# Optimization experiments

Measured on AMD Instinct MI355X. Metric: run time of the kernel, lower is better.

The kernel has to match this reference:

```python
import jax, jax.numpy as jnp
import numpy as np
from jax import lax

NX, NY = 6, 6
NB = NX * NY            # 36 blocks
B, S = 64, 256          # batch, sample_count
EPS = 1e-6

def build_edges(nx, ny):
    edges = []
    for i in range(nx):
        for j in range(ny):
            for dx, dy in [(-1, 0), (0, -1), (0, 1), (1, 0)]:
                x, y = i + dx, j + dy
                if 0 <= x < nx and 0 <= y < ny:
                    edges.append((j * nx + i, y * nx + x))
    return np.array(edges, np.int32)   # (120, 2)

EDGES_NP = build_edges(NX, NY)
NE = len(EDGES_NP)  # 120

def setup_inputs() -> dict:
    key = jax.random.key(0)
    ks = jax.random.split(key, 24)
    f32 = jnp.float32
    d = {
        "image":      jax.random.normal(ks[0], (B, 1, 32, 32), f32),
        "edge_noise": jax.random.uniform(ks[1], (B, S, NE), f32),
        "u_s":        jax.random.uniform(ks[2], (B, S, NB), f32),
        "u_d":        jax.random.uniform(ks[3], (B, S, NB), f32),
        # CNN params (OIHW)
        "cw1": jax.random.normal(ks[4], (32, 1, 5, 5), f32) * 0.05,
        "cb1": jnp.zeros((32,), f32),
        "cw2": jax.random.normal(ks[5], (32, 32, 5, 5), f32) * 0.05,
        "cb2": jnp.zeros((32,), f32),
        "cw3": jax.random.normal(ks[6], (64, 32, 5, 5), f32) * 0.05,
        "cb3": jnp.zeros((64,), f32),
        "cw4": jax.random.normal(ks[7], (64, 64, 5, 5), f32) * 0.05,
        "cb4": jnp.zeros((64,), f32),
        # is_connected MLP
        "wc1": jax.random.normal(ks[8], (256, 256), f32) * 0.05,
        "bc1": jnp.zeros((256,), f32),
        "wc2": jax.random.normal(ks[9], (256, NE), f32) * 0.05,
        "bc2": jnp.zeros((NE,), f32),
        # is_endpoint MLP
        "we1": jax.random.normal(ks[10], (256, 256), f32) * 0.05,
        "be1": jnp.zeros((256,), f32),
        "we2": jax.random.normal(ks[11], (256, NB), f32) * 0.05,
        "be2": jnp.zeros((NB,), f32),
        "edges": jnp.asarray(EDGES_NP),  # (NE, 2) int32, constants
    }
    return d

def _conv(x, w, b):
    y = lax.conv_general_dilated(x, w, (1, 1), 'VALID',
                                 dimension_numbers=('NCHW', 'OIHW', 'NCHW'))
    return y + b[None, :, None, None]

def _pool2(x):
    return lax.reduce_window(x, -jnp.inf, lax.max, (1, 1, 2, 2), (1, 1, 2, 2), 'VALID')

def reference(image, edge_noise, u_s, u_d,
              cw1, cb1, cw2, cb2, cw3, cb3, cw4, cb4,
              wc1, bc1, wc2, bc2, we1, be1, we2, be2, edges):
    # ---- CNN feature extractor ----
    h = _conv(image, cw1, cb1)
    h = _conv(h, cw2, cb2)
    h = _pool2(h)
    h = _conv(h, cw3, cb3)
    h = _conv(h, cw4, cb4)
    h = _pool2(h)
    emb = h.reshape(h.shape[0], -1)              # (B, 256)

    # ---- heads ----
    p_conn = jax.nn.sigmoid(jax.nn.relu(emb @ wc1 + bc1) @ wc2 + bc2)   # (B, NE)
    p_ep   = jax.nn.sigmoid(jax.nn.relu(emb @ we1 + be1) @ we2 + be2)   # (B, NB)

    pc = jnp.clip(p_conn, EPS, 1.0 - EPS)
    pe = jnp.clip(p_ep, EPS, 1.0 - EPS)
    cat = pe / pe.sum(-1, keepdims=True)
    logcat = jnp.log(cat)                        # (B, NB)

    # ---- Monte-Carlo sampling (ISED blackbox) ----
    conn = (edge_noise < pc[:, None, :]).astype(pc.dtype)               # (B,S,NE) Bernoulli
    g_s = -jnp.log(-jnp.log(jnp.clip(u_s, EPS, 1.0 - EPS)))
    g_d = -jnp.log(-jnp.log(jnp.clip(u_d, EPS, 1.0 - EPS)))
    s_idx = jnp.argmax(logcat[:, None, :] + g_s, axis=-1)               # (B,S) categorical
    d_idx = jnp.argmax(logcat[:, None, :] + g_d, axis=-1)               # (B,S)

    # ---- batched BFS reachability via boolean matrix squaring ----
    oh_u = jax.nn.one_hot(edges[:, 0], NB, dtype=pc.dtype)              # (NE, NB)
    oh_v = jax.nn.one_hot(edges[:, 1], NB, dtype=pc.dtype)
    e_sym = jnp.einsum('eu,ev->euv', oh_u, oh_v) + jnp.einsum('eu,ev->evu', oh_u, oh_v)
    A = jnp.minimum(jnp.einsum('bse,euv->bsuv', conn, e_sym), 1.0)      # (B,S,36,36)

    R = jnp.minimum(A + jnp.eye(NB, dtype=A.dtype), 1.0)
    for _ in range(6):                           # (I+A)^(2^6), covers path len<=36
        R = jnp.minimum(R @ R, 1.0)
    P = jnp.minimum(A @ R, 1.0)                  # paths of length >= 1 (BFS semantics)

    Pv = jnp.take_along_axis(P, s_idx[:, :, None, None], axis=2)[:, :, 0, :]  # (B,S,36)
    exists = (jnp.take_along_axis(Pv, d_idx[:, :, None], axis=2)[:, :, 0] > 0.5).astype(pc.dtype)  # (B,S)

    # ---- sample-probability weighting (differentiable ISED estimator) ----
    logw = (conn * jnp.log(pc)[:, None, :] + (1.0 - conn) * jnp.log1p(-pc)[:, None, :]).sum(-1)
    logw = logw + jnp.take_along_axis(logcat, s_idx, axis=1) \
                + jnp.take_along_axis(logcat, d_idx, axis=1)            # (B,S)
    w = jax.nn.softmax(logw, axis=1)
    p1 = (w * exists).sum(axis=1)                # P(path exists)
    return jnp.stack([1.0 - p1, p1], axis=-1)    # (B, 2)
```

## Files before the change

kernel.cpp:

```cpp
#include <hip/hip_runtime.h>

typedef unsigned long long u64;
#define EPSF 1e-6f

__global__ __launch_bounds__(512) void k_conv1(const float* __restrict__ img,
                                               const float* __restrict__ cw1,
                                               const float* __restrict__ cb1,
                                               float* __restrict__ c1) {
  int slab = blockIdx.x, b = blockIdx.y;
  __shared__ float simg[32 * 33];
  for (int k = threadIdx.x; k < 1024; k += 512) {
    int y = k >> 5, x = k & 31;
    simg[y * 33 + x] = img[b * 1024 + k];
  }
  int half = threadIdx.x >> 8;
  int u = threadIdx.x & 255;
  int ocl = u >> 5;
  int x = u & 31;
  int oc = slab * 8 + ocl;
  int y0 = half * 14;
  float w[25];
#pragma unroll
  for (int k = 0; k < 25; ++k) w[k] = cw1[oc * 25 + k];
  float bias = cb1[oc];
  __syncthreads();
  if (x < 28) {
    float acc[5];
#pragma unroll
    for (int k = 0; k < 5; ++k) acc[k] = bias;
    float* outp = c1 + (b * 32 + oc) * 784 + x;
#pragma unroll
    for (int rr = 0; rr < 18; ++rr) {
      int r = y0 + rr;
      float in[5];
#pragma unroll
      for (int c = 0; c < 5; ++c) in[c] = simg[r * 33 + x + c];
#pragma unroll
      for (int ky = 0; ky < 5; ++ky) {
        if (rr < ky || rr - ky > 13) continue;
        int slot = (rr - ky) % 5;
#pragma unroll
        for (int kx = 0; kx < 5; ++kx)
          acc[slot] = fmaf(w[ky * 5 + kx], in[kx], acc[slot]);
      }
      if (rr >= 4) {
        int slot = (rr - 4) % 5;
        outp[(y0 + rr - 4) * 28] = acc[slot];
        acc[slot] = bias;
      }
    }
  }
}

__global__ __launch_bounds__(1024, 4) void k_conv2(const float* __restrict__ c1,
                                                   const float* __restrict__ cw2,
                                                   const float* __restrict__ cb2,
                                                   float* __restrict__ p1w) {
  int ocq = blockIdx.x, b = blockIdx.y;
  __shared__ float smem[32384];
  float* w2s = smem + 25984;
  int t = threadIdx.x;
  {
    const float4* src = (const float4*)(cw2 + ocq * 8 * 800);
    for (int k4 = t; k4 < 1600; k4 += 1024) {
      float4 v = src[k4];
      float vv[4] = {v.x, v.y, v.z, v.w};
      int k = k4 * 4;
#pragma unroll
      for (int r = 0; r < 4; ++r) {
        int kk = k + r;
        int o = kk / 800, rest = kk % 800;
        w2s[rest * 8 + o] = vv[r];
      }
    }
  }
  if (t < 784) {
    int row = t / 28, col = t % 28;
    int lofs = row * 29 + col;
    const float* src = c1 + (size_t)b * 25088 + t;
#pragma unroll
    for (int ic = 0; ic < 32; ++ic) smem[ic * 812 + lofs] = src[ic * 784];
  }
  int w = __builtin_amdgcn_readfirstlane(t >> 6);
  int ocg = w & 1;
  int icq = w >> 1;
  int l = t & 63;
  int py = l >> 3, px = l & 7;
  int oc0 = ocq * 8 + ocg * 4;
  float acc[4][9];
#pragma unroll
  for (int o = 0; o < 4; ++o)
#pragma unroll
    for (int e = 0; e < 9; ++e) acc[o][e] = 0.f;
  __syncthreads();

  const float* base0 = smem + icq * 4 * 812 + (3 * py) * 29 + 3 * px;
  const float* wk0 = w2s + icq * 800 + ocg * 4;
#pragma unroll
  for (int icl = 0; icl < 4; ++icl) {
    const float* base = base0 + icl * 812;
    float win[7][7];
#pragma unroll
    for (int rr = 0; rr < 7; ++rr)
#pragma unroll
      for (int m = 0; m < 7; ++m) win[rr][m] = base[rr * 29 + m];
    const float* wk = wk0 + icl * 200;
#pragma unroll
    for (int ky = 0; ky < 5; ++ky) {
      float wq[5][4];
#pragma unroll
      for (int kx = 0; kx < 5; ++kx)
        *(float4*)wq[kx] = *(const float4*)(wk + (ky * 5 + kx) * 8);
#pragma unroll
      for (int i = 0; i < 3; ++i) {
#pragma unroll
        for (int kx = 0; kx < 5; ++kx) {
#pragma unroll
          for (int jj = 0; jj < 3; ++jj) {
            float v = win[i + ky][jj + kx];
            acc[0][i * 3 + jj] = fmaf(wq[kx][0], v, acc[0][i * 3 + jj]);
            acc[1][i * 3 + jj] = fmaf(wq[kx][1], v, acc[1][i * 3 + jj]);
            acc[2][i * 3 + jj] = fmaf(wq[kx][2], v, acc[2][i * 3 + jj]);
            acc[3][i * 3 + jj] = fmaf(wq[kx][3], v, acc[3][i * 3 + jj]);
          }
        }
      }
    }
  }

  __syncthreads();
  float* slots = smem;
  float* cbuf = smem + 18432;
  int chunk = ocg * 2304 + l * 9;
  if (icq >= 4) {
    float* d = slots + (icq - 4) * 4608 + chunk;
#pragma unroll
    for (int o = 0; o < 4; ++o)
#pragma unroll
      for (int e = 0; e < 9; ++e) d[o * 576 + e] = acc[o][e];
  }
  __syncthreads();
  if (icq < 4) {
    const float* s = slots + icq * 4608 + chunk;
#pragma unroll
    for (int o = 0; o < 4; ++o)
#pragma unroll
      for (int e = 0; e < 9; ++e) acc[o][e] += s[o * 576 + e];
  }
  __syncthreads();
  if (icq == 2 || icq == 3) {
    float* d = slots + (icq - 2) * 4608 + chunk;
#pragma unroll
    for (int o = 0; o < 4; ++o)
#pragma unroll
      for (int e = 0; e < 9; ++e) d[o * 576 + e] = acc[o][e];
  }
  __syncthreads();
  if (icq < 2) {
    const float* s = slots + icq * 4608 + chunk;
#pragma unroll
    for (int o = 0; o < 4; ++o)
#pragma unroll
      for (int e = 0; e < 9; ++e) acc[o][e] += s[o * 576 + e];
  }
  __syncthreads();
  if (icq == 1) {
    float* d = slots + chunk;
#pragma unroll
    for (int o = 0; o < 4; ++o)
#pragma unroll
      for (int e = 0; e < 9; ++e) d[o * 576 + e] = acc[o][e];
  }
  __syncthreads();
  if (icq == 0) {
    const float* s = slots + chunk;
#pragma unroll
    for (int o = 0; o < 4; ++o) {
      float bias = cb2[oc0 + o];
#pragma unroll
      for (int i = 0; i < 3; ++i)
#pragma unroll
        for (int jj = 0; jj < 3; ++jj)
          cbuf[(ocg * 4 + o) * 576 + (3 * py + i) * 24 + 3 * px + jj] =
              acc[o][i * 3 + jj] + s[o * 576 + i * 3 + jj] + bias;
    }
  }
  __syncthreads();
  for (int k = t; k < 1152; k += 1024) {
    int o = k / 144, rem = k % 144;
    int PY = rem / 12, PX = rem % 12;
    const float* b0 = cbuf + o * 576 + (2 * PY) * 24 + 2 * PX;
    float m = fmaxf(fmaxf(b0[0], b0[1]), fmaxf(b0[24], b0[25]));
    p1w[((size_t)b * 32 + ocq * 8 + o) * 144 + PY * 12 + PX] = m;
  }
}

__global__ __launch_bounds__(256) void k_conv3(const float* __restrict__ p1w,
                                               const float* __restrict__ cw3,
                                               const float* __restrict__ cb3,
                                               float* __restrict__ c3) {
  int oc8 = blockIdx.x, b = blockIdx.y;
  __shared__ float smem[11008];
  float* w3s = smem;
  float* ins = smem + 6400;
  int t = threadIdx.x;
  {
    const float4* src = (const float4*)(p1w + b * 32 * 144);
    float4* dst = (float4*)ins;
    for (int k = t; k < 1152; k += 256) dst[k] = src[k];
  }
  {
    const float4* src = (const float4*)(cw3 + oc8 * 8 * 800);
    for (int k4 = t; k4 < 1600; k4 += 256) {
      float4 v = src[k4];
      float vv[4] = {v.x, v.y, v.z, v.w};
      int k = k4 * 4;
#pragma unroll
      for (int r = 0; r < 4; ++r) {
        int kk = k + r;
        int o = kk / 800, rest = kk % 800;
        w3s[rest * 8 + o] = vv[r];
      }
    }
  }
  int g = t >> 4, p = t & 15;
  int ocg = p >> 3, row = p & 7;
  float acc[4][8];
#pragma unroll
  for (int j = 0; j < 4; ++j)
#pragma unroll
    for (int c = 0; c < 8; ++c) acc[j][c] = 0.f;
  __syncthreads();
#pragma unroll
  for (int icl = 0; icl < 2; ++icl) {
    int ic = g + icl * 16;
#pragma unroll
    for (int ky = 0; ky < 5; ++ky) {
      const float4* rp = (const float4*)(ins + ic * 144 + (row + ky) * 12);
      float win[12];
#pragma unroll
      for (int q = 0; q < 3; ++q) {
        float4 v = rp[q];
        win[4 * q] = v.x; win[4 * q + 1] = v.y; win[4 * q + 2] = v.z; win[4 * q + 3] = v.w;
      }
      const float* wb = w3s + (ic * 25 + ky * 5) * 8 + ocg * 4;
#pragma unroll
      for (int kx = 0; kx < 5; ++kx) {
        float wq[4];
        *(float4*)wq = *(const float4*)(wb + kx * 8);
#pragma unroll
        for (int c = 0; c < 8; ++c) {
#pragma unroll
          for (int j = 0; j < 4; ++j) acc[j][c] = fmaf(wq[j], win[c + kx], acc[j][c]);
        }
      }
    }
  }
  float* buf = smem;
  __syncthreads();
  if (g >= 8) {
    float* d = buf + (g - 8) * 512 + p * 32;
#pragma unroll
    for (int j = 0; j < 4; ++j)
#pragma unroll
      for (int c = 0; c < 8; ++c) d[j * 8 + c] = acc[j][c];
  }
  __syncthreads();
  if (g < 8) {
    const float* s = buf + g * 512 + p * 32;
#pragma unroll
    for (int j = 0; j < 4; ++j)
#pragma unroll
      for (int c = 0; c < 8; ++c) acc[j][c] += s[j * 8 + c];
  }
  __syncthreads();
  if (g >= 4 && g < 8) {
    float* d = buf + (g - 4) * 512 + p * 32;
#pragma unroll
    for (int j = 0; j < 4; ++j)
#pragma unroll
      for (int c = 0; c < 8; ++c) d[j * 8 + c] = acc[j][c];
  }
  __syncthreads();
  if (g < 4) {
    const float* s = buf + g * 512 + p * 32;
#pragma unroll
    for (int j = 0; j < 4; ++j)
#pragma unroll
      for (int c = 0; c < 8; ++c) acc[j][c] += s[j * 8 + c];
  }
  __syncthreads();
  if (g == 2 || g == 3) {
    float* d = buf + (g - 2) * 512 + p * 32;
#pragma unroll
    for (int j = 0; j < 4; ++j)
#pragma unroll
      for (int c = 0; c < 8; ++c) d[j * 8 + c] = acc[j][c];
  }
  __syncthreads();
  if (g < 2) {
    const float* s = buf + g * 512 + p * 32;
#pragma unroll
    for (int j = 0; j < 4; ++j)
#pragma unroll
      for (int c = 0; c < 8; ++c) acc[j][c] += s[j * 8 + c];
  }
  __syncthreads();
  if (g == 1) {
    float* d = buf + p * 32;
#pragma unroll
    for (int j = 0; j < 4; ++j)
#pragma unroll
      for (int c = 0; c < 8; ++c) d[j * 8 + c] = acc[j][c];
  }
  __syncthreads();
  if (g == 0) {
    const float* s = buf + p * 32;
#pragma unroll
    for (int j = 0; j < 4; ++j) {
      float bias = cb3[oc8 * 8 + ocg * 4 + j];
      float4 v0, v1;
      v0.x = acc[j][0] + s[j * 8 + 0] + bias; v0.y = acc[j][1] + s[j * 8 + 1] + bias;
      v0.z = acc[j][2] + s[j * 8 + 2] + bias; v0.w = acc[j][3] + s[j * 8 + 3] + bias;
      v1.x = acc[j][4] + s[j * 8 + 4] + bias; v1.y = acc[j][5] + s[j * 8 + 5] + bias;
      v1.z = acc[j][6] + s[j * 8 + 6] + bias; v1.w = acc[j][7] + s[j * 8 + 7] + bias;
      float* op = c3 + (b * 64 + oc8 * 8 + ocg * 4 + j) * 64 + row * 8;
      *(float4*)op = v0; *(float4*)(op + 4) = v1;
    }
  }
}

__global__ __launch_bounds__(256) void k_conv4(const float* __restrict__ c3,
                                               const float* __restrict__ cw4,
                                               const float* __restrict__ cb4,
                                               float* __restrict__ emb) {
  int oc8 = blockIdx.x, b = blockIdx.y;
  __shared__ float smem[17152];
  float* w4s = smem;
  float* ins = smem + 12800;
  int t = threadIdx.x;
  {
    const float4* src = (const float4*)(c3 + b * 4096);
    for (int k = t; k < 1024; k += 256) {
      int ic = k >> 4, q = k & 15;
      *(float4*)(ins + ic * 68 + q * 4) = src[k];
    }
  }
  {
    const float4* src = (const float4*)(cw4 + oc8 * 8 * 1600);
    for (int k4 = t; k4 < 3200; k4 += 256) {
      float4 v = src[k4];
      float vv[4] = {v.x, v.y, v.z, v.w};
      int k = k4 * 4;
#pragma unroll
      for (int r = 0; r < 4; ++r) {
        int kk = k + r;
        int o = kk / 1600, rest = kk % 1600;
        w4s[rest * 8 + o] = vv[r];
      }
    }
  }
  int g = t >> 3, p = t & 7;
  int ocg = p >> 2, row = p & 3;
  float acc[4][4];
#pragma unroll
  for (int j = 0; j < 4; ++j)
#pragma unroll
    for (int c = 0; c < 4; ++c) acc[j][c] = 0.f;
  __syncthreads();
#pragma unroll
  for (int icl = 0; icl < 2; ++icl) {
    int ic = g + icl * 32;
#pragma unroll
    for (int ky = 0; ky < 5; ++ky) {
      const float4* rp = (const float4*)(ins + ic * 68 + (row + ky) * 8);
      float win[8];
#pragma unroll
      for (int q = 0; q < 2; ++q) {
        float4 v = rp[q];
        win[4 * q] = v.x; win[4 * q + 1] = v.y; win[4 * q + 2] = v.z; win[4 * q + 3] = v.w;
      }
      const float* wb = w4s + (ic * 25 + ky * 5) * 8 + ocg * 4;
#pragma unroll
      for (int kx = 0; kx < 5; ++kx) {
        float wq[4];
        *(float4*)wq = *(const float4*)(wb + kx * 8);
#pragma unroll
        for (int c = 0; c < 4; ++c) {
#pragma unroll
          for (int j = 0; j < 4; ++j) acc[j][c] = fmaf(wq[j], win[c + kx], acc[j][c]);
        }
      }
    }
  }
  float* buf = smem;
#pragma unroll
  for (int half = 16; half >= 1; half >>= 1) {
    __syncthreads();
    if (g >= half && g < 2 * half) {
      float* d = buf + (g - half) * 128 + p * 16;
#pragma unroll
      for (int j = 0; j < 4; ++j)
#pragma unroll
        for (int c = 0; c < 4; ++c) d[j * 4 + c] = acc[j][c];
    }
    __syncthreads();
    if (g < half) {
      const float* s = buf + g * 128 + p * 16;
#pragma unroll
      for (int j = 0; j < 4; ++j)
#pragma unroll
        for (int c = 0; c < 4; ++c) acc[j][c] += s[j * 4 + c];
    }
  }
  float* pb = buf + 2048;
  if (g == 0) {
#pragma unroll
    for (int j = 0; j < 4; ++j) {
      float bias = cb4[oc8 * 8 + ocg * 4 + j];
#pragma unroll
      for (int c = 0; c < 4; ++c) pb[(ocg * 4 + j) * 16 + row * 4 + c] = acc[j][c] + bias;
    }
  }
  __syncthreads();
  if (t < 32) {
    int o = t >> 2, q = t & 3, py = q >> 1, px = q & 1;
    const float* b0 = pb + o * 16 + (2 * py) * 4 + 2 * px;
    float m = fmaxf(fmaxf(b0[0], b0[1]), fmaxf(b0[4], b0[5]));
    emb[b * 256 + (oc8 * 8 + o) * 4 + py * 2 + px] = m;
  }
}

__global__ __launch_bounds__(256) void k_heads(const float* __restrict__ emb,
    const float* __restrict__ wc1, const float* __restrict__ bc1,
    const float* __restrict__ wc2, const float* __restrict__ bc2,
    const float* __restrict__ we1, const float* __restrict__ be1,
    const float* __restrict__ we2, const float* __restrict__ be2,
    float* __restrict__ pcw, float* __restrict__ lpcw,
    float* __restrict__ l1mw, float* __restrict__ lcatw) {
  int head = blockIdx.x, b = blockIdx.y;
  int t = threadIdx.x;
  __shared__ float e_s[256], h_s[256];
  __shared__ float aux;
  e_s[t] = emb[b * 256 + t];
  __syncthreads();
  const float* W1 = head ? we1 : wc1;
  const float* B1 = head ? be1 : bc1;
  float s = B1[t];
  for (int i = 0; i < 256; i += 4) {
    s = fmaf(e_s[i], W1[i * 256 + t], s);
    s = fmaf(e_s[i + 1], W1[(i + 1) * 256 + t], s);
    s = fmaf(e_s[i + 2], W1[(i + 2) * 256 + t], s);
    s = fmaf(e_s[i + 3], W1[(i + 3) * 256 + t], s);
  }
  h_s[t] = fmaxf(s, 0.f);
  __syncthreads();
  int NO = head ? 36 : 120;
  const float* W2 = head ? we2 : wc2;
  const float* B2 = head ? be2 : bc2;
  if (t < NO) {
    float s2 = B2[t];
    for (int i = 0; i < 256; ++i) s2 = fmaf(h_s[i], W2[i * NO + t], s2);
    float p = 1.f / (1.f + expf(-s2));
    p = fminf(fmaxf(p, EPSF), 1.f - EPSF);
    if (head == 0) {
      pcw[b * 120 + t] = p;
      lpcw[b * 120 + t] = logf(p);
      l1mw[b * 120 + t] = log1pf(-p);
    } else {
      e_s[t] = p;
    }
  }
  if (head == 1) {
    __syncthreads();
    if (t == 0) {
      float sm = 0.f;
      for (int j2 = 0; j2 < 36; ++j2) sm += e_s[j2];
      aux = sm;
    }
    __syncthreads();
    if (t < 36) lcatw[b * 36 + t] = logf(e_s[t] / aux);
  }
}

__global__ __launch_bounds__(64) void k_mc1(const float* __restrict__ enoise,
    const float* __restrict__ us, const float* __restrict__ ud,
    const int* __restrict__ edges,
    const float* __restrict__ pcw, const float* __restrict__ lpcw,
    const float* __restrict__ l1mw, const float* __restrict__ lcatw,
    float* __restrict__ lw, float* __restrict__ exx) {
  int chunk = blockIdx.x, b = blockIdx.y, t = threadIdx.x;
  int s = chunk * 64 + t;
  __shared__ __align__(16) float pc_s[120];
  __shared__ __align__(16) float lpc_s[120];
  __shared__ __align__(16) float l1m_s[120];
  __shared__ __align__(16) float lcat_s[36];
  __shared__ __align__(16) int einfo[120];
  for (int k = t; k < 120; k += 64) {
    pc_s[k] = pcw[b * 120 + k];
    lpc_s[k] = lpcw[b * 120 + k];
    l1m_s[k] = l1mw[b * 120 + k];
    int u = edges[2 * k], v = edges[2 * k + 1];
    int d = v - u;
    int isV = (d == 6 || d == -6) ? 1 : 0;
    int pos = d > 0 ? u : v;
    einfo[k] = pos | (isV << 6);
  }
  if (t < 36) lcat_s[t] = lcatw[b * 36 + t];
  __syncthreads();

  float logw = 0.f;
  u64 H = 0, V = 0;
  {
    const float4* np = (const float4*)(enoise + ((size_t)(b * 256 + s)) * 120);
#pragma unroll
    for (int q = 0; q < 30; ++q) {
      float4 nz = np[q];
      float4 p4 = ((const float4*)pc_s)[q];
      float4 lp4 = ((const float4*)lpc_s)[q];
      float4 lm4 = ((const float4*)l1m_s)[q];
      int4 e4 = ((const int4*)einfo)[q];
      float nv[4] = {nz.x, nz.y, nz.z, nz.w};
      float pv[4] = {p4.x, p4.y, p4.z, p4.w};
      float lv[4] = {lp4.x, lp4.y, lp4.z, lp4.w};
      float mv[4] = {lm4.x, lm4.y, lm4.z, lm4.w};
      int ev[4] = {e4.x, e4.y, e4.z, e4.w};
#pragma unroll
      for (int r = 0; r < 4; ++r) {
        bool conn = nv[r] < pv[r];
        logw += conn ? lv[r] : mv[r];
        if (conn) {
          u64 bit = 1ull << (ev[r] & 63);
          if (ev[r] & 64) V |= bit; else H |= bit;
        }
      }
    }
  }
  int si = 0, di = 0;
  {
    const float4* up = (const float4*)(us + ((size_t)(b * 256 + s)) * 36);
    float best = -1e30f;
#pragma unroll
    for (int q = 0; q < 9; ++q) {
      float4 uv = up[q];
      float4 lc4 = ((const float4*)lcat_s)[q];
      float vv[4] = {uv.x, uv.y, uv.z, uv.w};
      float lc[4] = {lc4.x, lc4.y, lc4.z, lc4.w};
#pragma unroll
      for (int r = 0; r < 4; ++r) {
        float u = fminf(fmaxf(vv[r], EPSF), 1.f - EPSF);
        float gq = -logf(-logf(u));
        float val = lc[r] + gq;
        if (val > best) { best = val; si = q * 4 + r; }
      }
    }
  }
  {
    const float4* up = (const float4*)(ud + ((size_t)(b * 256 + s)) * 36);
    float best = -1e30f;
#pragma unroll
    for (int q = 0; q < 9; ++q) {
      float4 uv = up[q];
      float4 lc4 = ((const float4*)lcat_s)[q];
      float vv[4] = {uv.x, uv.y, uv.z, uv.w};
      float lc[4] = {lc4.x, lc4.y, lc4.z, lc4.w};
#pragma unroll
      for (int r = 0; r < 4; ++r) {
        float u = fminf(fmaxf(vv[r], EPSF), 1.f - EPSF);
        float gq = -logf(-logf(u));
        float val = lc[r] + gq;
        if (val > best) { best = val; di = q * 4 + r; }
      }
    }
  }
  logw += lcat_s[si] + lcat_s[di];

  u64 comp = 1ull << si;
  while (true) {
    u64 prev = comp;
    comp |= ((comp & H) << 1) | ((comp >> 1) & H);
    comp |= ((comp & V) << 6) | ((comp >> 6) & V);
    if (comp == prev) break;
  }
  float ex;
  if (si == di) ex = (comp != (1ull << si)) ? 1.f : 0.f;
  else ex = ((comp >> di) & 1ull) ? 1.f : 0.f;

  lw[b * 256 + s] = logw;
  exx[b * 256 + s] = ex;
}

__global__ __launch_bounds__(256) void k_mc2(const float* __restrict__ lw,
                                             const float* __restrict__ exx,
                                             float* __restrict__ out) {
  int b = blockIdx.x, t = threadIdx.x;
  __shared__ float red_s[256];
  float logw = lw[b * 256 + t];
  float ex = exx[b * 256 + t];
  red_s[t] = logw; __syncthreads();
  for (int off = 128; off > 0; off >>= 1) {
    if (t < off) red_s[t] = fmaxf(red_s[t], red_s[t + off]);
    __syncthreads();
  }
  float m = red_s[0]; __syncthreads();
  float evx = expf(logw - m);
  red_s[t] = evx; __syncthreads();
  for (int off = 128; off > 0; off >>= 1) {
    if (t < off) red_s[t] += red_s[t + off];
    __syncthreads();
  }
  float den = red_s[0]; __syncthreads();
  red_s[t] = evx * ex; __syncthreads();
  for (int off = 128; off > 0; off >>= 1) {
    if (t < off) red_s[t] += red_s[t + off];
    __syncthreads();
  }
  if (t == 0) {
    float p1v = red_s[0] / den;
    out[b * 2] = 1.f - p1v;
    out[b * 2 + 1] = p1v;
  }
}

extern "C" void kernel_launch(void* const* d_in, const int* in_sizes, int n_in,
                              void* d_out, int out_size, void* d_ws, size_t ws_size,
                              hipStream_t stream) {
  const float* image = (const float*)d_in[0];
  const float* enoise = (const float*)d_in[1];
  const float* us = (const float*)d_in[2];
  const float* udn = (const float*)d_in[3];
  const float* cw1 = (const float*)d_in[4];
  const float* cb1 = (const float*)d_in[5];
  const float* cw2 = (const float*)d_in[6];
  const float* cb2 = (const float*)d_in[7];
  const float* cw3 = (const float*)d_in[8];
  const float* cb3 = (const float*)d_in[9];
  const float* cw4 = (const float*)d_in[10];
  const float* cb4 = (const float*)d_in[11];
  const float* wc1 = (const float*)d_in[12];
  const float* bc1 = (const float*)d_in[13];
  const float* wc2 = (const float*)d_in[14];
  const float* bc2 = (const float*)d_in[15];
  const float* we1 = (const float*)d_in[16];
  const float* be1 = (const float*)d_in[17];
  const float* we2 = (const float*)d_in[18];
  const float* be2 = (const float*)d_in[19];
  const int* edges = (const int*)d_in[20];

  float* ws = (float*)d_ws;
  float* c1 = ws;
  float* p1w = ws + 1605632;
  float* c3 = ws + 1900544;
  float* emb = ws + 2162688;
  float* pcw = ws + 2179072;
  float* lpcw = ws + 2186752;
  float* l1mw = ws + 2194432;
  float* lcatw = ws + 2202112;
  float* lw = ws + 2204416;
  float* exx = ws + 2220800;
  float* outp = (float*)d_out;

  k_conv1<<<dim3(4, 64), dim3(512), 0, stream>>>(image, cw1, cb1, c1);
  k_conv2<<<dim3(4, 64), dim3(1024), 0, stream>>>(c1, cw2, cb2, p1w);
  k_conv3<<<dim3(8, 64), dim3(256), 0, stream>>>(p1w, cw3, cb3, c3);
  k_conv4<<<dim3(8, 64), dim3(256), 0, stream>>>(c3, cw4, cb4, emb);
  k_heads<<<dim3(2, 64), dim3(256), 0, stream>>>(emb, wc1, bc1, wc2, bc2,
                                                 we1, be1, we2, be2,
                                                 pcw, lpcw, l1mw, lcatw);
  k_mc1<<<dim3(4, 64), dim3(64), 0, stream>>>(enoise, us, udn, edges,
                                              pcw, lpcw, l1mw, lcatw, lw, exx);
  k_mc2<<<dim3(64), dim3(256), 0, stream>>>(lw, exx, outp);
}
```

Before: 119.6 us.

## Fuse conv1 into conv2 and merge heads with Monte Carlo stages into one tail kernel

Conv1 is now computed directly into conv2's shared-memory input tile, so the conv1 output no longer makes a round trip through global memory. Each conv2 block recomputes the full conv1 for its image, which is redundant across the four output-channel blocks. The two MLP heads, the per-sample path check and the softmax reduction are merged into one 64-block kernel, removing three launches and the intermediate global buffers. The cost is lower parallelism in the tail, since the heads now run serially per batch element on only 64 blocks.

After: 130.4 us. 1.09x slower.

```diff
diff --git a/kernel.cpp b/kernel.cpp
--- a/kernel.cpp
+++ b/kernel.cpp
@@ -3,63 +3,21 @@
 typedef unsigned long long u64;
 #define EPSF 1e-6f
 
-__global__ __launch_bounds__(512) void k_conv1(const float* __restrict__ img,
-                                               const float* __restrict__ cw1,
-                                               const float* __restrict__ cb1,
-                                               float* __restrict__ c1) {
-  int slab = blockIdx.x, b = blockIdx.y;
-  __shared__ float simg[32 * 33];
-  for (int k = threadIdx.x; k < 1024; k += 512) {
-    int y = k >> 5, x = k & 31;
-    simg[y * 33 + x] = img[b * 1024 + k];
-  }
-  int half = threadIdx.x >> 8;
-  int u = threadIdx.x & 255;
-  int ocl = u >> 5;
-  int x = u & 31;
-  int oc = slab * 8 + ocl;
-  int y0 = half * 14;
-  float w[25];
-#pragma unroll
-  for (int k = 0; k < 25; ++k) w[k] = cw1[oc * 25 + k];
-  float bias = cb1[oc];
-  __syncthreads();
-  if (x < 28) {
-    float acc[5];
-#pragma unroll
-    for (int k = 0; k < 5; ++k) acc[k] = bias;
-    float* outp = c1 + (b * 32 + oc) * 784 + x;
-#pragma unroll
-    for (int rr = 0; rr < 18; ++rr) {
-      int r = y0 + rr;
-      float in[5];
-#pragma unroll
-      for (int c = 0; c < 5; ++c) in[c] = simg[r * 33 + x + c];
-#pragma unroll
-      for (int ky = 0; ky < 5; ++ky) {
-        if (rr < ky || rr - ky > 13) continue;
-        int slot = (rr - ky) % 5;
-#pragma unroll
-        for (int kx = 0; kx < 5; ++kx)
-          acc[slot] = fmaf(w[ky * 5 + kx], in[kx], acc[slot]);
-      }
-      if (rr >= 4) {
-        int slot = (rr - 4) % 5;
-        outp[(y0 + rr - 4) * 28] = acc[slot];
-        acc[slot] = bias;
-      }
-    }
-  }
-}
-
-__global__ __launch_bounds__(1024, 4) void k_conv2(const float* __restrict__ c1,
+__global__ __launch_bounds__(1024, 4) void k_conv2(const float* __restrict__ img,
+                                                   const float* __restrict__ cw1,
+                                                   const float* __restrict__ cb1,
                                                    const float* __restrict__ cw2,
                                                    const float* __restrict__ cb2,
                                                    float* __restrict__ p1w) {
   int ocq = blockIdx.x, b = blockIdx.y;
-  __shared__ float smem[32384];
+  __shared__ float smem[33440];
   float* w2s = smem + 25984;
+  float* simg = smem + 32384;
   int t = threadIdx.x;
+  if (t < 1024) {
+    int y = t >> 5, x = t & 31;
+    simg[y * 33 + x] = img[b * 1024 + t];
+  }
   {
     const float4* src = (const float4*)(cw2 + ocq * 8 * 800);
     for (int k4 = t; k4 < 1600; k4 += 1024) {
@@ -74,12 +32,36 @@
       }
     }
   }
-  if (t < 784) {
-    int row = t / 28, col = t % 28;
-    int lofs = row * 29 + col;
-    const float* src = c1 + (size_t)b * 25088 + t;
-#pragma unroll
-    for (int ic = 0; ic < 32; ++ic) smem[ic * 812 + lofs] = src[ic * 784];
+  __syncthreads();
+  if (t < 896) {
+    int ic = t / 28, x = t % 28;
+    float w1[25];
+#pragma unroll
+    for (int k = 0; k < 25; ++k) w1[k] = cw1[ic * 25 + k];
+    float bias = cb1[ic];
+    float acc[5];
+#pragma unroll
+    for (int k = 0; k < 5; ++k) acc[k] = bias;
+    float* orow = smem + ic * 812 + x;
+#pragma unroll
+    for (int rr = 0; rr < 32; ++rr) {
+      float in[5];
+#pragma unroll
+      for (int c = 0; c < 5; ++c) in[c] = simg[rr * 33 + x + c];
+#pragma unroll
+      for (int ky = 0; ky < 5; ++ky) {
+        if (rr < ky || rr - ky > 27) continue;
+        int slot = (rr - ky) % 5;
+#pragma unroll
+        for (int kx = 0; kx < 5; ++kx)
+          acc[slot] = fmaf(w1[ky * 5 + kx], in[kx], acc[slot]);
+      }
+      if (rr >= 4) {
+        int slot = (rr - 4) % 5;
+        orow[(rr - 4) * 29] = acc[slot];
+        acc[slot] = bias;
+      }
+    }
   }
   int w = __builtin_amdgcn_readfirstlane(t >> 6);
   int ocg = w & 1;
@@ -431,88 +413,85 @@
   }
 }
 
-__global__ __launch_bounds__(256) void k_heads(const float* __restrict__ emb,
+__global__ __launch_bounds__(256) void k_tail(const float* __restrict__ emb,
     const float* __restrict__ wc1, const float* __restrict__ bc1,
     const float* __restrict__ wc2, const float* __restrict__ bc2,
     const float* __restrict__ we1, const float* __restrict__ be1,
     const float* __restrict__ we2, const float* __restrict__ be2,
-    float* __restrict__ pcw, float* __restrict__ lpcw,
-    float* __restrict__ l1mw, float* __restrict__ lcatw) {
-  int head = blockIdx.x, b = blockIdx.y;
-  int t = threadIdx.x;
+    const float* __restrict__ enoise, const float* __restrict__ us,
+    const float* __restrict__ ud, const int* __restrict__ edges,
+    float* __restrict__ out) {
+  int b = blockIdx.x, t = threadIdx.x;
   __shared__ float e_s[256], h_s[256];
-  __shared__ float aux;
-  e_s[t] = emb[b * 256 + t];
-  __syncthreads();
-  const float* W1 = head ? we1 : wc1;
-  const float* B1 = head ? be1 : bc1;
-  float s = B1[t];
-  for (int i = 0; i < 256; i += 4) {
-    s = fmaf(e_s[i], W1[i * 256 + t], s);
-    s = fmaf(e_s[i + 1], W1[(i + 1) * 256 + t], s);
-    s = fmaf(e_s[i + 2], W1[(i + 2) * 256 + t], s);
-    s = fmaf(e_s[i + 3], W1[(i + 3) * 256 + t], s);
-  }
-  h_s[t] = fmaxf(s, 0.f);
-  __syncthreads();
-  int NO = head ? 36 : 120;
-  const float* W2 = head ? we2 : wc2;
-  const float* B2 = head ? be2 : bc2;
-  if (t < NO) {
-    float s2 = B2[t];
-    for (int i = 0; i < 256; ++i) s2 = fmaf(h_s[i], W2[i * NO + t], s2);
-    float p = 1.f / (1.f + expf(-s2));
-    p = fminf(fmaxf(p, EPSF), 1.f - EPSF);
-    if (head == 0) {
-      pcw[b * 120 + t] = p;
-      lpcw[b * 120 + t] = logf(p);
-      l1mw[b * 120 + t] = log1pf(-p);
-    } else {
-      e_s[t] = p;
-    }
-  }
-  if (head == 1) {
-    __syncthreads();
-    if (t == 0) {
-      float sm = 0.f;
-      for (int j2 = 0; j2 < 36; ++j2) sm += e_s[j2];
-      aux = sm;
-    }
-    __syncthreads();
-    if (t < 36) lcatw[b * 36 + t] = logf(e_s[t] / aux);
-  }
-}
-
-__global__ __launch_bounds__(64) void k_mc1(const float* __restrict__ enoise,
-    const float* __restrict__ us, const float* __restrict__ ud,
-    const int* __restrict__ edges,
-    const float* __restrict__ pcw, const float* __restrict__ lpcw,
-    const float* __restrict__ l1mw, const float* __restrict__ lcatw,
-    float* __restrict__ lw, float* __restrict__ exx) {
-  int chunk = blockIdx.x, b = blockIdx.y, t = threadIdx.x;
-  int s = chunk * 64 + t;
   __shared__ __align__(16) float pc_s[120];
   __shared__ __align__(16) float lpc_s[120];
   __shared__ __align__(16) float l1m_s[120];
   __shared__ __align__(16) float lcat_s[36];
   __shared__ __align__(16) int einfo[120];
-  for (int k = t; k < 120; k += 64) {
-    pc_s[k] = pcw[b * 120 + k];
-    lpc_s[k] = lpcw[b * 120 + k];
-    l1m_s[k] = l1mw[b * 120 + k];
-    int u = edges[2 * k], v = edges[2 * k + 1];
+  __shared__ float red_s[256];
+  __shared__ float aux;
+  e_s[t] = emb[b * 256 + t];
+  if (t < 120) {
+    int u = edges[2 * t], v = edges[2 * t + 1];
     int d = v - u;
     int isV = (d == 6 || d == -6) ? 1 : 0;
     int pos = d > 0 ? u : v;
-    einfo[k] = pos | (isV << 6);
-  }
-  if (t < 36) lcat_s[t] = lcatw[b * 36 + t];
+    einfo[t] = pos | (isV << 6);
+  }
+  __syncthreads();
+  {
+    float s = bc1[t];
+    for (int i = 0; i < 256; i += 4) {
+      s = fmaf(e_s[i], wc1[i * 256 + t], s);
+      s = fmaf(e_s[i + 1], wc1[(i + 1) * 256 + t], s);
+      s = fmaf(e_s[i + 2], wc1[(i + 2) * 256 + t], s);
+      s = fmaf(e_s[i + 3], wc1[(i + 3) * 256 + t], s);
+    }
+    h_s[t] = fmaxf(s, 0.f);
+  }
+  __syncthreads();
+  if (t < 120) {
+    float s2 = bc2[t];
+    for (int i = 0; i < 256; ++i) s2 = fmaf(h_s[i], wc2[i * 120 + t], s2);
+    float p = 1.f / (1.f + expf(-s2));
+    p = fminf(fmaxf(p, EPSF), 1.f - EPSF);
+    pc_s[t] = p;
+    lpc_s[t] = logf(p);
+    l1m_s[t] = log1pf(-p);
+  }
+  __syncthreads();
+  {
+    float s = be1[t];
+    for (int i = 0; i < 256; i += 4) {
+      s = fmaf(e_s[i], we1[i * 256 + t], s);
+      s = fmaf(e_s[i + 1], we1[(i + 1) * 256 + t], s);
+      s = fmaf(e_s[i + 2], we1[(i + 2) * 256 + t], s);
+      s = fmaf(e_s[i + 3], we1[(i + 3) * 256 + t], s);
+    }
+    h_s[t] = fmaxf(s, 0.f);
+  }
+  __syncthreads();
+  if (t < 36) {
+    float s2 = be2[t];
+    for (int i = 0; i < 256; ++i) s2 = fmaf(h_s[i], we2[i * 36 + t], s2);
+    float p = 1.f / (1.f + expf(-s2));
+    p = fminf(fmaxf(p, EPSF), 1.f - EPSF);
+    red_s[t] = p;
+  }
+  __syncthreads();
+  if (t == 0) {
+    float sm = 0.f;
+    for (int j = 0; j < 36; ++j) sm += red_s[j];
+    aux = sm;
+  }
+  __syncthreads();
+  if (t < 36) lcat_s[t] = logf(red_s[t] / aux);
   __syncthreads();
 
   float logw = 0.f;
   u64 H = 0, V = 0;
   {
-    const float4* np = (const float4*)(enoise + ((size_t)(b * 256 + s)) * 120);
+    const float4* np = (const float4*)(enoise + ((size_t)(b * 256 + t)) * 120);
 #pragma unroll
     for (int q = 0; q < 30; ++q) {
       float4 nz = np[q];
@@ -538,7 +517,7 @@
   }
   int si = 0, di = 0;
   {
-    const float4* up = (const float4*)(us + ((size_t)(b * 256 + s)) * 36);
+    const float4* up = (const float4*)(us + ((size_t)(b * 256 + t)) * 36);
     float best = -1e30f;
 #pragma unroll
     for (int q = 0; q < 9; ++q) {
@@ -556,7 +535,7 @@
     }
   }
   {
-    const float4* up = (const float4*)(ud + ((size_t)(b * 256 + s)) * 36);
+    const float4* up = (const float4*)(ud + ((size_t)(b * 256 + t)) * 36);
     float best = -1e30f;
 #pragma unroll
     for (int q = 0; q < 9; ++q) {
@@ -586,17 +565,7 @@
   if (si == di) ex = (comp != (1ull << si)) ? 1.f : 0.f;
   else ex = ((comp >> di) & 1ull) ? 1.f : 0.f;
 
-  lw[b * 256 + s] = logw;
-  exx[b * 256 + s] = ex;
-}
-
-__global__ __launch_bounds__(256) void k_mc2(const float* __restrict__ lw,
-                                             const float* __restrict__ exx,
-                                             float* __restrict__ out) {
-  int b = blockIdx.x, t = threadIdx.x;
-  __shared__ float red_s[256];
-  float logw = lw[b * 256 + t];
-  float ex = exx[b * 256 + t];
+  __syncthreads();
   red_s[t] = logw; __syncthreads();
   for (int off = 128; off > 0; off >>= 1) {
     if (t < off) red_s[t] = fmaxf(red_s[t], red_s[t + off]);
@@ -648,26 +617,15 @@
   const int* edges = (const int*)d_in[20];
 
   float* ws = (float*)d_ws;
-  float* c1 = ws;
-  float* p1w = ws + 1605632;
-  float* c3 = ws + 1900544;
-  float* emb = ws + 2162688;
-  float* pcw = ws + 2179072;
-  float* lpcw = ws + 2186752;
-  float* l1mw = ws + 2194432;
-  float* lcatw = ws + 2202112;
-  float* lw = ws + 2204416;
-  float* exx = ws + 2220800;
+  float* p1w = ws;
+  float* c3 = ws + 294912;
+  float* emb = ws + 557056;
   float* outp = (float*)d_out;
 
-  k_conv1<<<dim3(4, 64), dim3(512), 0, stream>>>(image, cw1, cb1, c1);
-  k_conv2<<<dim3(4, 64), dim3(1024), 0, stream>>>(c1, cw2, cb2, p1w);
+  k_conv2<<<dim3(4, 64), dim3(1024), 0, stream>>>(image, cw1, cb1, cw2, cb2, p1w);
   k_conv3<<<dim3(8, 64), dim3(256), 0, stream>>>(p1w, cw3, cb3, c3);
   k_conv4<<<dim3(8, 64), dim3(256), 0, stream>>>(c3, cw4, cb4, emb);
-  k_heads<<<dim3(2, 64), dim3(256), 0, stream>>>(emb, wc1, bc1, wc2, bc2,
-                                                 we1, be1, we2, be2,
-                                                 pcw, lpcw, l1mw, lcatw);
-  k_mc1<<<dim3(4, 64), dim3(64), 0, stream>>>(enoise, us, udn, edges,
-                                              pcw, lpcw, l1mw, lcatw, lw, exx);
-  k_mc2<<<dim3(64), dim3(256), 0, stream>>>(lw, exx, outp);
+  k_tail<<<dim3(64), dim3(256), 0, stream>>>(emb, wc1, bc1, wc2, bc2,
+                                             we1, be1, we2, be2,
+                                             enoise, us, udn, edges, outp);
 }
```

## Fuse conv1 into conv2 via shared memory and stage MC inputs in LDS

Applied to the files above, without the earlier changes.

Conv1 no longer runs as its own kernel. Each conv2 block recomputes the full 32-channel conv1 output for its image directly into shared memory, which removes one launch and the global write and read of the 6.4 MB c1 tensor. The cost is that conv1 is recomputed four times, once per oc-quarter block, and shared memory per block grows. Separately, k_mc1 now loads the edge noise and uniform samples with coalesced float4 reads into padded LDS tiles instead of strided per-thread global reads.

Result: slower. 126.0 us (+5.4%).

```diff
diff --git a/kernel.cpp b/kernel.cpp
--- a/kernel.cpp
+++ b/kernel.cpp
@@ -3,63 +3,21 @@
 typedef unsigned long long u64;
 #define EPSF 1e-6f
 
-__global__ __launch_bounds__(512) void k_conv1(const float* __restrict__ img,
-                                               const float* __restrict__ cw1,
-                                               const float* __restrict__ cb1,
-                                               float* __restrict__ c1) {
-  int slab = blockIdx.x, b = blockIdx.y;
-  __shared__ float simg[32 * 33];
-  for (int k = threadIdx.x; k < 1024; k += 512) {
-    int y = k >> 5, x = k & 31;
-    simg[y * 33 + x] = img[b * 1024 + k];
-  }
-  int half = threadIdx.x >> 8;
-  int u = threadIdx.x & 255;
-  int ocl = u >> 5;
-  int x = u & 31;
-  int oc = slab * 8 + ocl;
-  int y0 = half * 14;
-  float w[25];
-#pragma unroll
-  for (int k = 0; k < 25; ++k) w[k] = cw1[oc * 25 + k];
-  float bias = cb1[oc];
-  __syncthreads();
-  if (x < 28) {
-    float acc[5];
-#pragma unroll
-    for (int k = 0; k < 5; ++k) acc[k] = bias;
-    float* outp = c1 + (b * 32 + oc) * 784 + x;
-#pragma unroll
-    for (int rr = 0; rr < 18; ++rr) {
-      int r = y0 + rr;
-      float in[5];
-#pragma unroll
-      for (int c = 0; c < 5; ++c) in[c] = simg[r * 33 + x + c];
-#pragma unroll
-      for (int ky = 0; ky < 5; ++ky) {
-        if (rr < ky || rr - ky > 13) continue;
-        int slot = (rr - ky) % 5;
-#pragma unroll
-        for (int kx = 0; kx < 5; ++kx)
-          acc[slot] = fmaf(w[ky * 5 + kx], in[kx], acc[slot]);
-      }
-      if (rr >= 4) {
-        int slot = (rr - 4) % 5;
-        outp[(y0 + rr - 4) * 28] = acc[slot];
-        acc[slot] = bias;
-      }
-    }
-  }
-}
-
-__global__ __launch_bounds__(1024, 4) void k_conv2(const float* __restrict__ c1,
+__global__ __launch_bounds__(1024, 4) void k_conv2(const float* __restrict__ img,
+                                                   const float* __restrict__ cw1,
+                                                   const float* __restrict__ cb1,
                                                    const float* __restrict__ cw2,
                                                    const float* __restrict__ cb2,
                                                    float* __restrict__ p1w) {
   int ocq = blockIdx.x, b = blockIdx.y;
-  __shared__ float smem[32384];
+  __shared__ float smem[33440];
   float* w2s = smem + 25984;
+  float* simg = smem + 32384;
   int t = threadIdx.x;
+  if (t < 1024) {
+    int y = t >> 5, x = t & 31;
+    simg[y * 33 + x] = img[b * 1024 + t];
+  }
   {
     const float4* src = (const float4*)(cw2 + ocq * 8 * 800);
     for (int k4 = t; k4 < 1600; k4 += 1024) {
@@ -74,12 +32,36 @@
       }
     }
   }
-  if (t < 784) {
-    int row = t / 28, col = t % 28;
-    int lofs = row * 29 + col;
-    const float* src = c1 + (size_t)b * 25088 + t;
-#pragma unroll
-    for (int ic = 0; ic < 32; ++ic) smem[ic * 812 + lofs] = src[ic * 784];
+  __syncthreads();
+  if (t < 896) {
+    int ic = t / 28, x = t % 28;
+    float w1[25];
+#pragma unroll
+    for (int k = 0; k < 25; ++k) w1[k] = cw1[ic * 25 + k];
+    float bias = cb1[ic];
+    float acc[5];
+#pragma unroll
+    for (int k = 0; k < 5; ++k) acc[k] = bias;
+    float* orow = smem + ic * 812 + x;
+#pragma unroll
+    for (int rr = 0; rr < 32; ++rr) {
+      float in[5];
+#pragma unroll
+      for (int c = 0; c < 5; ++c) in[c] = simg[rr * 33 + x + c];
+#pragma unroll
+      for (int ky = 0; ky < 5; ++ky) {
+        if (rr < ky || rr - ky > 27) continue;
+        int slot = (rr - ky) % 5;
+#pragma unroll
+        for (int kx = 0; kx < 5; ++kx)
+          acc[slot] = fmaf(w1[ky * 5 + kx], in[kx], acc[slot]);
+      }
+      if (rr >= 4) {
+        int slot = (rr - 4) % 5;
+        orow[(rr - 4) * 29] = acc[slot];
+        acc[slot] = bias;
+      }
+    }
   }
   int w = __builtin_amdgcn_readfirstlane(t >> 6);
   int ocg = w & 1;
@@ -490,7 +472,9 @@
     const float* __restrict__ l1mw, const float* __restrict__ lcatw,
     float* __restrict__ lw, float* __restrict__ exx) {
   int chunk = blockIdx.x, b = blockIdx.y, t = threadIdx.x;
-  int s = chunk * 64 + t;
+  __shared__ __align__(16) float en_s[64 * 124];
+  __shared__ __align__(16) float us_s[64 * 40];
+  __shared__ __align__(16) float ud_s[64 * 40];
   __shared__ __align__(16) float pc_s[120];
   __shared__ __align__(16) float lpc_s[120];
   __shared__ __align__(16) float l1m_s[120];
@@ -507,12 +491,36 @@
     einfo[k] = pos | (isV << 6);
   }
   if (t < 36) lcat_s[t] = lcatw[b * 36 + t];
+  {
+    const float4* src = (const float4*)(enoise + ((size_t)(b * 256 + chunk * 64)) * 120);
+    for (int k = t; k < 1920; k += 64) {
+      float4 v = src[k];
+      int s = k / 30, e4 = k % 30;
+      *(float4*)(en_s + s * 124 + e4 * 4) = v;
+    }
+  }
+  {
+    const float4* src = (const float4*)(us + ((size_t)(b * 256 + chunk * 64)) * 36);
+    for (int k = t; k < 576; k += 64) {
+      float4 v = src[k];
+      int s = k / 9, e4 = k % 9;
+      *(float4*)(us_s + s * 40 + e4 * 4) = v;
+    }
+  }
+  {
+    const float4* src = (const float4*)(ud + ((size_t)(b * 256 + chunk * 64)) * 36);
+    for (int k = t; k < 576; k += 64) {
+      float4 v = src[k];
+      int s = k / 9, e4 = k % 9;
+      *(float4*)(ud_s + s * 40 + e4 * 4) = v;
+    }
+  }
   __syncthreads();
 
   float logw = 0.f;
   u64 H = 0, V = 0;
   {
-    const float4* np = (const float4*)(enoise + ((size_t)(b * 256 + s)) * 120);
+    const float4* np = (const float4*)(en_s + t * 124);
 #pragma unroll
     for (int q = 0; q < 30; ++q) {
       float4 nz = np[q];
@@ -538,7 +546,7 @@
   }
   int si = 0, di = 0;
   {
-    const float4* up = (const float4*)(us + ((size_t)(b * 256 + s)) * 36);
+    const float4* up = (const float4*)(us_s + t * 40);
     float best = -1e30f;
 #pragma unroll
     for (int q = 0; q < 9; ++q) {
@@ -556,7 +564,7 @@
     }
   }
   {
-    const float4* up = (const float4*)(ud + ((size_t)(b * 256 + s)) * 36);
+    const float4* up = (const float4*)(ud_s + t * 40);
     float best = -1e30f;
 #pragma unroll
     for (int q = 0; q < 9; ++q) {
@@ -586,6 +594,7 @@
   if (si == di) ex = (comp != (1ull << si)) ? 1.f : 0.f;
   else ex = ((comp >> di) & 1ull) ? 1.f : 0.f;
 
+  int s = chunk * 64 + t;
   lw[b * 256 + s] = logw;
   exx[b * 256 + s] = ex;
 }
@@ -648,20 +657,18 @@
   const int* edges = (const int*)d_in[20];
 
   float* ws = (float*)d_ws;
-  float* c1 = ws;
-  float* p1w = ws + 1605632;
-  float* c3 = ws + 1900544;
-  float* emb = ws + 2162688;
-  float* pcw = ws + 2179072;
-  float* lpcw = ws + 2186752;
-  float* l1mw = ws + 2194432;
-  float* lcatw = ws + 2202112;
-  float* lw = ws + 2204416;
-  float* exx = ws + 2220800;
+  float* p1w = ws;
+  float* c3 = ws + 294912;
+  float* emb = ws + 557056;
+  float* pcw = ws + 573440;
+  float* lpcw = ws + 581120;
+  float* l1mw = ws + 588800;
+  float* lcatw = ws + 596480;
+  float* lw = ws + 598784;
+  float* exx = ws + 615168;
   float* outp = (float*)d_out;
 
-  k_conv1<<<dim3(4, 64), dim3(512), 0, stream>>>(image, cw1, cb1, c1);
-  k_conv2<<<dim3(4, 64), dim3(1024), 0, stream>>>(c1, cw2, cb2, p1w);
+  k_conv2<<<dim3(4, 64), dim3(1024), 0, stream>>>(image, cw1, cb1, cw2, cb2, p1w);
   k_conv3<<<dim3(8, 64), dim3(256), 0, stream>>>(p1w, cw3, cb3, c3);
   k_conv4<<<dim3(8, 64), dim3(256), 0, stream>>>(c3, cw4, cb4, emb);
   k_heads<<<dim3(2, 64), dim3(256), 0, stream>>>(emb, wc1, bc1, wc2, bc2,
```
